# Kernel optimization log

Measured on AMD Instinct MI355X. Metric: run time of the kernel, lower is better.

The kernel has to match this reference:

```python
import jax, jax.numpy as jnp
import numpy as np

N_NODES = 20000

def gcn(h, W, b, src, dst):
    # DGL GraphConv, norm='both': D_out^-1/2 on src, aggregate, D_in^-1/2 on dst, then W, b
    E = src.shape[0]
    ones = jnp.ones((E,), dtype=h.dtype)
    out_deg = jnp.clip(jax.ops.segment_sum(ones, src, N_NODES), 1.0)
    in_deg = jnp.clip(jax.ops.segment_sum(ones, dst, N_NODES), 1.0)
    dn_src = jax.lax.rsqrt(out_deg)  # [N]
    dn_dst = jax.lax.rsqrt(in_deg)
    hs = h * dn_src[None, :, None]           # [B,N,H]
    msg = hs[:, src, :]                      # [B,E,H] gather
    agg = jax.vmap(lambda m: jax.ops.segment_sum(m, dst, N_NODES))(msg)  # [B,N,H]
    agg = agg * dn_dst[None, :, None]
    return agg @ W + b

def setup_inputs() -> dict:
    key = jax.random.key(0)
    ks = jax.random.split(key, 16)
    B, N, H, I, E = 4, N_NODES, 128, 64, 320000
    inp = {
        'x': jax.random.normal(ks[0], (B, I), jnp.float32),
        'h_prev': jax.random.normal(ks[1], (B, N, H), jnp.float32),
        'c_prev': jax.random.normal(ks[2], (B, N, H), jnp.float32),
        'src': jax.random.randint(ks[3], (E,), 0, N, jnp.int32),
        'dst': jax.random.randint(ks[4], (E,), 0, N, jnp.int32),
    }
    s_in = 1.0 / np.sqrt(I)
    s_h = 1.0 / np.sqrt(H)
    inp['Wi'] = jax.random.uniform(ks[5], (I, H), jnp.float32, -s_in, s_in)
    inp['bi'] = jax.random.uniform(ks[6], (H,), jnp.float32, -s_in, s_in)
    inp['Wf'] = jax.random.uniform(ks[7], (I, H), jnp.float32, -s_in, s_in)
    inp['bf'] = jax.random.uniform(ks[8], (H,), jnp.float32, -s_in, s_in)
    inp['Wo'] = jax.random.uniform(ks[9], (I, H), jnp.float32, -s_in, s_in)
    inp['bo'] = jax.random.uniform(ks[10], (H,), jnp.float32, -s_in, s_in)
    inp['Wc'] = jax.random.uniform(ks[11], (I, H), jnp.float32, -s_in, s_in)
    inp['bc'] = jax.random.uniform(ks[12], (H,), jnp.float32, -s_in, s_in)
    inp['Wg'] = jax.random.uniform(ks[13], (H, H), jnp.float32, -s_h, s_h)
    inp['bg'] = jax.random.uniform(ks[14], (H,), jnp.float32, -s_h, s_h)
    return inp

def reference(x, h_prev, c_prev, src, dst, Wi, bi, Wf, bf, Wo, bo, Wc, bc, Wg, bg):
    # gcn_h(g, h_prev) is identical in all four gates -> compute once
    gh = gcn(h_prev, Wg, bg, src, dst)  # [B,N,H]
    i_t = jax.nn.sigmoid((x @ Wi + bi)[:, None, :] + gh)
    f_t = jax.nn.sigmoid((x @ Wf + bf)[:, None, :] + gh)
    o_t = jax.nn.sigmoid((x @ Wo + bo)[:, None, :] + gh)
    c_tilde = jnp.tanh((x @ Wc + bc)[:, None, :] + gh)
    c_t = f_t * c_prev + i_t * c_tilde
    h_t = o_t * jnp.tanh(c_t)
    return h_t, c_t
```

## Files before the change

kernel.cpp:

```cpp
#include <hip/hip_runtime.h>
#include <hip/hip_bf16.h>

#define N_NODES 20000
#define B 4
#define H 128
#define I_DIM 64
#define E_MAX 320000
#define CAP 64

__device__ int   g_cnt_dst[N_NODES];
__device__ int   g_deg_src[N_NODES];
__device__ int   g_csr[N_NODES * CAP];
__device__ float g_xg[4 * B * H];
__device__ uint2 g_hs[N_NODES * H];

__global__ __launch_bounds__(256)
void degree_kernel(const int* __restrict__ src, int E, int eb,
                   const float* __restrict__ x,
                   const float* __restrict__ Wi, const float* __restrict__ bi,
                   const float* __restrict__ Wf, const float* __restrict__ bf_,
                   const float* __restrict__ Wo, const float* __restrict__ bo,
                   const float* __restrict__ Wc, const float* __restrict__ bc) {
    int blk = blockIdx.x;
    int t = threadIdx.x;
    if (blk < eb) {
        int e = blk * 256 + t;
        if (e < E) atomicAdd(&g_deg_src[src[e]], 1);
    } else {
        int bid = blk - eb;
        int g = bid >> 1;
        int b = ((bid & 1) << 1) | (t >> 7);
        int h = t & 127;
        const float* W;
        const float* bb;
        switch (g) {
            case 0: W = Wi; bb = bi; break;
            case 1: W = Wf; bb = bf_; break;
            case 2: W = Wo; bb = bo; break;
            default: W = Wc; bb = bc; break;
        }
        float acc = bb[h];
#pragma unroll
        for (int i = 0; i < I_DIM; i++)
            acc += x[b * I_DIM + i] * W[i * H + h];
        g_xg[(g * B + b) * H + h] = acc;
    }
}

__global__ __launch_bounds__(256)
void mid_kernel(const float* __restrict__ h_prev,
                const int* __restrict__ src, const int* __restrict__ dst, int E) {
    const int PACK_BLKS = (N_NODES * H) / 256;
    int blk = blockIdx.x;
    int t = threadIdx.x;

    if (blk < PACK_BLKS) {
        int i = blk * 256 + t;
        int n = i >> 7;
        float sc = rsqrtf(fmaxf((float)g_deg_src[n], 1.0f));
        const long stride = (long)N_NODES * H;
        float v0 = h_prev[i] * sc;
        float v1 = h_prev[i + stride] * sc;
        float v2 = h_prev[i + 2 * stride] * sc;
        float v3 = h_prev[i + 3 * stride] * sc;
        __hip_bfloat162 p01 = __float22bfloat162_rn(make_float2(v0, v1));
        __hip_bfloat162 p23 = __float22bfloat162_rn(make_float2(v2, v3));
        uint2 wv;
        wv.x = *reinterpret_cast<unsigned int*>(&p01);
        wv.y = *reinterpret_cast<unsigned int*>(&p23);
        g_hs[i] = wv;
    } else {
        int e = (blk - PACK_BLKS) * 256 + t;
        if (e < E) {
            int d = dst[e];
            int slot = atomicAdd(&g_cnt_dst[d], 1);
            if (slot < CAP) g_csr[(d << 6) + slot] = src[e];
        }
    }
}

__device__ __forceinline__ float fast_sigmoid(float z) {
    return 1.f / (1.f + __expf(-z));
}
__device__ __forceinline__ float fast_tanh(float z) {
    return 1.f - 2.f / (__expf(2.f * z) + 1.f);
}

__global__ __launch_bounds__(128)
void fused_kernel(const float* __restrict__ Wg, const float* __restrict__ bg,
                  const float* __restrict__ c_prev,
                  float* __restrict__ out_h, float* __restrict__ out_c) {
    int n = blockIdx.x;
    int h = threadIdx.x;
    int cnt = g_cnt_dst[n];
    float dd = rsqrtf(fmaxf((float)cnt, 1.0f));
    if (cnt > CAP) cnt = CAP;
    int beg = n << 6;

    __shared__ int sbase[CAP];
    if (h < CAP) {
        int s = g_csr[beg + (h < cnt ? h : 0)];
        sbase[h] = s << 7;
    }
    __syncthreads();

    float a0 = 0.f, a1 = 0.f, a2 = 0.f, a3 = 0.f;

#define ACC(w) { \
        __hip_bfloat162 p01 = *reinterpret_cast<__hip_bfloat162*>(&(w).x); \
        __hip_bfloat162 p23 = *reinterpret_cast<__hip_bfloat162*>(&(w).y); \
        float2 f01 = __bfloat1622float2(p01); \
        float2 f23 = __bfloat1622float2(p23); \
        a0 += f01.x; a1 += f01.y; a2 += f23.x; a3 += f23.y; }

    int j = 0;
    for (; j + 8 <= cnt; j += 8) {
        int b0 = sbase[j];
        int b1 = sbase[j + 1];
        int b2 = sbase[j + 2];
        int b3 = sbase[j + 3];
        int b4 = sbase[j + 4];
        int b5 = sbase[j + 5];
        int b6 = sbase[j + 6];
        int b7 = sbase[j + 7];
        uint2 w0 = g_hs[b0 + h];
        uint2 w1 = g_hs[b1 + h];
        uint2 w2 = g_hs[b2 + h];
        uint2 w3 = g_hs[b3 + h];
        uint2 w4 = g_hs[b4 + h];
        uint2 w5 = g_hs[b5 + h];
        uint2 w6 = g_hs[b6 + h];
        uint2 w7 = g_hs[b7 + h];
        ACC(w0); ACC(w1); ACC(w2); ACC(w3);
        ACC(w4); ACC(w5); ACC(w6); ACC(w7);
    }
    for (; j + 4 <= cnt; j += 4) {
        int b0 = sbase[j];
        int b1 = sbase[j + 1];
        int b2 = sbase[j + 2];
        int b3 = sbase[j + 3];
        uint2 w0 = g_hs[b0 + h];
        uint2 w1 = g_hs[b1 + h];
        uint2 w2 = g_hs[b2 + h];
        uint2 w3 = g_hs[b3 + h];
        ACC(w0); ACC(w1); ACC(w2); ACC(w3);
    }
    for (; j < cnt; j++) {
        uint2 w = g_hs[sbase[j] + h];
        ACC(w);
    }
#undef ACC

    __shared__ float4 arow4[H];
    arow4[h] = make_float4(a0 * dd, a1 * dd, a2 * dd, a3 * dd);
    __syncthreads();

    float g0 = 0.f, g1 = 0.f, g2 = 0.f, g3 = 0.f;
#pragma unroll 8
    for (int k = 0; k < H; k++) {
        float w = Wg[k * H + h];
        float4 a = arow4[k];
        g0 += a.x * w;
        g1 += a.y * w;
        g2 += a.z * w;
        g3 += a.w * w;
    }
    float bgh = bg[h];

    const long stride = (long)N_NODES * H;
    float gh_arr[B] = {g0 + bgh, g1 + bgh, g2 + bgh, g3 + bgh};
#pragma unroll
    for (int b = 0; b < B; b++) {
        float gh = gh_arr[b];
        float xi = g_xg[(0 * B + b) * H + h];
        float xf = g_xg[(1 * B + b) * H + h];
        float xo = g_xg[(2 * B + b) * H + h];
        float xc = g_xg[(3 * B + b) * H + h];

        float it = fast_sigmoid(xi + gh);
        float ft = fast_sigmoid(xf + gh);
        float ot = fast_sigmoid(xo + gh);
        float ct = fast_tanh(xc + gh);

        long idx = (long)b * stride + (long)n * H + h;
        float cp = c_prev[idx];
        float c  = ft * cp + it * ct;
        float ho = ot * fast_tanh(c);

        out_h[idx] = ho;
        out_c[idx] = c;
    }

    if (h == 0)  g_cnt_dst[n] = 0;
    if (h == 64) g_deg_src[n] = 0;
}

extern "C" void kernel_launch(void* const* d_in, const int* in_sizes, int n_in,
                              void* d_out, int out_size, void* d_ws, size_t ws_size,
                              hipStream_t stream) {
    const float* x      = (const float*)d_in[0];
    const float* h_prev = (const float*)d_in[1];
    const float* c_prev = (const float*)d_in[2];
    const int* src = (const int*)d_in[3];
    const int* dst = (const int*)d_in[4];
    const float* Wi = (const float*)d_in[5];
    const float* bi = (const float*)d_in[6];
    const float* Wf = (const float*)d_in[7];
    const float* bf_ = (const float*)d_in[8];
    const float* Wo = (const float*)d_in[9];
    const float* bo = (const float*)d_in[10];
    const float* Wc = (const float*)d_in[11];
    const float* bc = (const float*)d_in[12];
    const float* Wg = (const float*)d_in[13];
    const float* bg = (const float*)d_in[14];

    int E = in_sizes[3];
    if (E > E_MAX) E = E_MAX;
    int eb = (E + 255) / 256;
    const int PACK_BLKS = (N_NODES * H) / 256;

    degree_kernel<<<eb + 8, 256, 0, stream>>>(src, E, eb,
        x, Wi, bi, Wf, bf_, Wo, bo, Wc, bc);
    mid_kernel<<<PACK_BLKS + eb, 256, 0, stream>>>(h_prev, src, dst, E);

    float* out_h = (float*)d_out;
    float* out_c = out_h + (long)B * N_NODES * H;
    fused_kernel<<<N_NODES, 128, 0, stream>>>(Wg, bg, c_prev, out_h, out_c);
}
```

Baseline: 305.0 us.

## Process two nodes per block, use readlane for half of Wg matvec, nontemporal IO

The fused kernel now handles two destination nodes per 256-thread block. For the half of the feature dimension a wave already owns, it takes the aggregated row values by cross-lane readlane instead of reading them back from LDS, and reads only the other half from shared memory. c_prev is loaded early with nontemporal loads so the memory access overlaps the gather, and the outputs are written with nontemporal stores to avoid polluting the cache. The aim is to cut LDS traffic and block count and to hide global memory latency, at the cost of more registers and a block-wide sync shared across two nodes with unequal degrees.

```diff
diff --git a/kernel.cpp b/kernel.cpp
--- a/kernel.cpp
+++ b/kernel.cpp
@@ -86,43 +86,54 @@
     return 1.f - 2.f / (__expf(2.f * z) + 1.f);
 }
 
-__global__ __launch_bounds__(128)
+__global__ __launch_bounds__(256)
 void fused_kernel(const float* __restrict__ Wg, const float* __restrict__ bg,
                   const float* __restrict__ c_prev,
                   float* __restrict__ out_h, float* __restrict__ out_c) {
-    int n = blockIdx.x;
-    int h = threadIdx.x;
+    int t = threadIdx.x;
+    int ni = t >> 7;
+    int h = t & 127;
+    int w = (t >> 6) & 1;
+    int lane = t & 63;
+    int n = (blockIdx.x << 1) + ni;
+
     int cnt = g_cnt_dst[n];
     float dd = rsqrtf(fmaxf((float)cnt, 1.0f));
     if (cnt > CAP) cnt = CAP;
-    int beg = n << 6;
-
-    __shared__ int sbase[CAP];
-    if (h < CAP) {
-        int s = g_csr[beg + (h < cnt ? h : 0)];
-        sbase[h] = s << 7;
+
+    const long stride = (long)N_NODES * H;
+    float cp[B];
+#pragma unroll
+    for (int b = 0; b < B; b++)
+        cp[b] = __builtin_nontemporal_load(&c_prev[(long)b * stride + (long)n * H + h]);
+
+    __shared__ int sbase[2][CAP];
+    if (h < 64) {
+        int s = g_csr[(n << 6) + (lane < cnt ? lane : 0)];
+        sbase[ni][lane] = s << 7;
     }
     __syncthreads();
 
     float a0 = 0.f, a1 = 0.f, a2 = 0.f, a3 = 0.f;
 
-#define ACC(w) { \
-        __hip_bfloat162 p01 = *reinterpret_cast<__hip_bfloat162*>(&(w).x); \
-        __hip_bfloat162 p23 = *reinterpret_cast<__hip_bfloat162*>(&(w).y); \
+#define ACC(wv) { \
+        __hip_bfloat162 p01 = *reinterpret_cast<__hip_bfloat162*>(&(wv).x); \
+        __hip_bfloat162 p23 = *reinterpret_cast<__hip_bfloat162*>(&(wv).y); \
         float2 f01 = __bfloat1622float2(p01); \
         float2 f23 = __bfloat1622float2(p23); \
         a0 += f01.x; a1 += f01.y; a2 += f23.x; a3 += f23.y; }
 
+    const int* sb = sbase[ni];
     int j = 0;
     for (; j + 8 <= cnt; j += 8) {
-        int b0 = sbase[j];
-        int b1 = sbase[j + 1];
-        int b2 = sbase[j + 2];
-        int b3 = sbase[j + 3];
-        int b4 = sbase[j + 4];
-        int b5 = sbase[j + 5];
-        int b6 = sbase[j + 6];
-        int b7 = sbase[j + 7];
+        int b0 = sb[j];
+        int b1 = sb[j + 1];
+        int b2 = sb[j + 2];
+        int b3 = sb[j + 3];
+        int b4 = sb[j + 4];
+        int b5 = sb[j + 5];
+        int b6 = sb[j + 6];
+        int b7 = sb[j + 7];
         uint2 w0 = g_hs[b0 + h];
         uint2 w1 = g_hs[b1 + h];
         uint2 w2 = g_hs[b2 + h];
@@ -135,10 +146,10 @@
         ACC(w4); ACC(w5); ACC(w6); ACC(w7);
     }
     for (; j + 4 <= cnt; j += 4) {
-        int b0 = sbase[j];
-        int b1 = sbase[j + 1];
-        int b2 = sbase[j + 2];
-        int b3 = sbase[j + 3];
+        int b0 = sb[j];
+        int b1 = sb[j + 1];
+        int b2 = sb[j + 2];
+        int b3 = sb[j + 3];
         uint2 w0 = g_hs[b0 + h];
         uint2 w1 = g_hs[b1 + h];
         uint2 w2 = g_hs[b2 + h];
@@ -146,28 +157,44 @@
         ACC(w0); ACC(w1); ACC(w2); ACC(w3);
     }
     for (; j < cnt; j++) {
-        uint2 w = g_hs[sbase[j] + h];
-        ACC(w);
+        uint2 wv = g_hs[sb[j] + h];
+        ACC(wv);
     }
 #undef ACC
 
-    __shared__ float4 arow4[H];
-    arow4[h] = make_float4(a0 * dd, a1 * dd, a2 * dd, a3 * dd);
+    a0 *= dd; a1 *= dd; a2 *= dd; a3 *= dd;
+
+    __shared__ float4 arow4[2][H];
+    arow4[ni][h] = make_float4(a0, a1, a2, a3);
     __syncthreads();
 
     float g0 = 0.f, g1 = 0.f, g2 = 0.f, g3 = 0.f;
+
 #pragma unroll 8
-    for (int k = 0; k < H; k++) {
-        float w = Wg[k * H + h];
-        float4 a = arow4[k];
-        g0 += a.x * w;
-        g1 += a.y * w;
-        g2 += a.z * w;
-        g3 += a.w * w;
-    }
+    for (int kk = 0; kk < 64; kk++) {
+        int k = (w << 6) + kk;
+        float wv = Wg[k * H + h];
+        float b0 = __int_as_float(__builtin_amdgcn_readlane(__float_as_int(a0), kk));
+        float b1 = __int_as_float(__builtin_amdgcn_readlane(__float_as_int(a1), kk));
+        float b2 = __int_as_float(__builtin_amdgcn_readlane(__float_as_int(a2), kk));
+        float b3 = __int_as_float(__builtin_amdgcn_readlane(__float_as_int(a3), kk));
+        g0 += b0 * wv;
+        g1 += b1 * wv;
+        g2 += b2 * wv;
+        g3 += b3 * wv;
+    }
+#pragma unroll 8
+    for (int kk = 0; kk < 64; kk++) {
+        int k = ((1 - w) << 6) + kk;
+        float4 a = arow4[ni][k];
+        float wv = Wg[k * H + h];
+        g0 += a.x * wv;
+        g1 += a.y * wv;
+        g2 += a.z * wv;
+        g3 += a.w * wv;
+    }
+
     float bgh = bg[h];
-
-    const long stride = (long)N_NODES * H;
     float gh_arr[B] = {g0 + bgh, g1 + bgh, g2 + bgh, g3 + bgh};
 #pragma unroll
     for (int b = 0; b < B; b++) {
@@ -182,13 +209,12 @@
         float ot = fast_sigmoid(xo + gh);
         float ct = fast_tanh(xc + gh);
 
+        float c  = ft * cp[b] + it * ct;
+        float ho = ot * fast_tanh(c);
+
         long idx = (long)b * stride + (long)n * H + h;
-        float cp = c_prev[idx];
-        float c  = ft * cp + it * ct;
-        float ho = ot * fast_tanh(c);
-
-        out_h[idx] = ho;
-        out_c[idx] = c;
+        __builtin_nontemporal_store(ho, &out_h[idx]);
+        __builtin_nontemporal_store(c,  &out_c[idx]);
     }
 
     if (h == 0)  g_cnt_dst[n] = 0;
@@ -225,5 +251,5 @@
 
     float* out_h = (float*)d_out;
     float* out_c = out_h + (long)B * N_NODES * H;
-    fused_kernel<<<N_NODES, 128, 0, stream>>>(Wg, bg, c_prev, out_h, out_c);
-}
+    fused_kernel<<<N_NODES / 2, 256, 0, stream>>>(Wg, bg, c_prev, out_h, out_c);
+}
```

Measured after the change: 315.3 us. 1.03x slower.
